# Kernel tuning notes

Hardware: AMD Instinct MI355X
Metric: run time of the kernel (lower is better)

## Reference

```python
import jax, jax.numpy as jnp
import numpy as np

N_NODES = 3_000_000  # divisible by 3 (x.view(-1, 3))
N_EDGES = 48_000_000  # avg degree 16


def setup_inputs() -> dict:
    key = jax.random.key(0)
    ks = jax.random.split(key, 8)
    x = jax.random.normal(ks[0], (N_NODES, 1), dtype=jnp.float32)
    edge_index = jax.random.randint(ks[1], (2, N_EDGES), 0, N_NODES, dtype=jnp.int64)
    # SAGEConv(1, 1, bias=False): lin_l applied to aggregated neighbors, lin_r to root
    W_l = jax.random.normal(ks[2], (1, 1), dtype=jnp.float32)
    W_r = jax.random.normal(ks[3], (1, 1), dtype=jnp.float32)
    # nn.Sequential(Linear(1,2), ReLU, Linear(2,1)) with default biases
    W1 = jax.random.normal(ks[4], (2, 1), dtype=jnp.float32)
    b1 = jax.random.normal(ks[5], (2,), dtype=jnp.float32)
    W2 = jax.random.normal(ks[6], (1, 2), dtype=jnp.float32)
    b2 = jax.random.normal(ks[7], (1,), dtype=jnp.float32)
    return {"x": x, "edge_index": edge_index, "W_l": W_l, "W_r": W_r,
            "W1": W1, "b1": b1, "W2": W2, "b2": b2}


def reference(x, edge_index, W_l, W_r, W1, b1, W2, b2):
    src, dst = edge_index[0], edge_index[1]
    # sum-aggregate messages x_j from source nodes onto target nodes
    agg = jax.ops.segment_sum(x[src], dst, num_segments=N_NODES)  # [N, 1]
    # SAGEConv: lin_l(agg) + lin_r(x)
    h = agg @ W_l.T + x @ W_r.T  # [N, 1]
    # x.view(-1, 3)[:, 0] -> take every 3rd node's feature
    h0 = h.reshape(-1, 3)[:, 0:1]  # [N/3, 1]
    # MLP: Linear(1,2) -> ReLU -> Linear(2,1)
    out = jax.nn.relu(h0 @ W1.T + b1) @ W2.T + b2  # [N/3, 1]
    return out.reshape(-1)
```

## Files before the change

kernel.cpp:

```cpp
#include <hip/hip_runtime.h>


static constexpr int kNodes = 3000000;
static constexpr int kEdges = 48000000;
static constexpr int kOut   = 1000000;

static constexpr int RANGE_LOG = 12;
static constexpr int RANGE     = 1 << RANGE_LOG;
static constexpr int NBINS     = (kOut + RANGE - 1) / RANGE;
static constexpr int NBINS_PAD = 256;
static constexpr int CAP       = 71680;

static constexpr int K1_THREADS = 512;
static constexpr int E_PER_ITER = K1_THREADS * 8;
static constexpr int K1_ITERS   = 16;
static constexpr int E_PER_WG   = E_PER_ITER * K1_ITERS;
static constexpr int K1_GRID    = (kEdges + E_PER_WG - 1) / E_PER_WG;

__global__ __launch_bounds__(512) void scatter_bin3(
    const int* __restrict__ ei,
    const float* __restrict__ x,
    unsigned* __restrict__ count,
    uint2* __restrict__ recs)
{
    __shared__ unsigned hist[NBINS_PAD];
    __shared__ unsigned cur[NBINS_PAD];

    const int tid = threadIdx.x;
    if (tid < NBINS_PAD) hist[tid] = 0;
    __syncthreads();

    const int wgBase = blockIdx.x * E_PER_WG;

    for (int it = 0; it < K1_ITERS; ++it) {
        const int e = wgBase + it * E_PER_ITER + tid * 8;
        if (e < kEdges) {
            const int4 d0 = *reinterpret_cast<const int4*>(ei + kEdges + e);
            const int4 d1 = *reinterpret_cast<const int4*>(ei + kEdges + e + 4);
            const int dd[8] = {d0.x, d0.y, d0.z, d0.w, d1.x, d1.y, d1.z, d1.w};
#pragma unroll
            for (int k = 0; k < 8; ++k) {
                const unsigned d = (unsigned)dd[k];
                const unsigned q = d / 3u;
                if (q * 3u == d) {
                    atomicAdd(&hist[q >> RANGE_LOG], 1u);
                }
            }
        }
    }
    __syncthreads();

    if (tid < NBINS_PAD) {
        const unsigned c = hist[tid];
        unsigned base = 0;
        if (c) base = atomicAdd(&count[tid], c);
        cur[tid] = (unsigned)tid * (unsigned)CAP + base;
    }
    __syncthreads();

    for (int it = 0; it < K1_ITERS; ++it) {
        const int e = wgBase + it * E_PER_ITER + tid * 8;
        if (e < kEdges) {
            const int4 s0 = *reinterpret_cast<const int4*>(ei + e);
            const int4 s1 = *reinterpret_cast<const int4*>(ei + e + 4);
            const int4 d0 = *reinterpret_cast<const int4*>(ei + kEdges + e);
            const int4 d1 = *reinterpret_cast<const int4*>(ei + kEdges + e + 4);

            const int ss[8] = {s0.x, s0.y, s0.z, s0.w, s1.x, s1.y, s1.z, s1.w};
            const int dd[8] = {d0.x, d0.y, d0.z, d0.w, d1.x, d1.y, d1.z, d1.w};

#pragma unroll
            for (int h = 0; h < 2; ++h) {
                unsigned qv[4]; bool ok[4]; float xv[4];
#pragma unroll
                for (int k = 0; k < 4; ++k) {
                    const unsigned d = (unsigned)dd[h * 4 + k];
                    const unsigned q = d / 3u;
                    qv[k] = q;
                    ok[k] = (q * 3u == d);
                    xv[k] = ok[k] ? x[ss[h * 4 + k]] : 0.0f;
                }
#pragma unroll
                for (int k = 0; k < 4; ++k) {
                    if (ok[k]) {
                        const unsigned bin = qv[k] >> RANGE_LOG;
                        const unsigned pos = atomicAdd(&cur[bin], 1u);
                        if (pos < (bin + 1u) * (unsigned)CAP) {
                            uint2 r;
                            r.x = qv[k] & (unsigned)(RANGE - 1);
                            r.y = __float_as_uint(xv[k]);
                            recs[pos] = r;
                        }
                    }
                }
            }
        }
    }
}

__global__ __launch_bounds__(1024) void bin_finalize3(
    const unsigned* __restrict__ count,
    const uint2* __restrict__ recs,
    const float* __restrict__ x,
    const float* __restrict__ Wl,
    const float* __restrict__ Wr,
    const float* __restrict__ W1,
    const float* __restrict__ b1,
    const float* __restrict__ W2,
    const float* __restrict__ b2,
    float* __restrict__ out)
{
    __shared__ float acc[RANGE];

    const int tid = threadIdx.x;
    const int b   = blockIdx.x;

    for (int l = tid; l < RANGE; l += 1024) acc[l] = 0.0f;
    __syncthreads();

    unsigned cnt = count[b];
    if (cnt > (unsigned)CAP) cnt = CAP;
    const uint2* rb = recs + (size_t)b * CAP;

    unsigned i = (unsigned)tid;
    for (; i + 3072u < cnt; i += 4096u) {
        const uint2 r0 = rb[i];
        const uint2 r1 = rb[i + 1024u];
        const uint2 r2 = rb[i + 2048u];
        const uint2 r3 = rb[i + 3072u];
        atomicAdd(&acc[r0.x], __uint_as_float(r0.y));
        atomicAdd(&acc[r1.x], __uint_as_float(r1.y));
        atomicAdd(&acc[r2.x], __uint_as_float(r2.y));
        atomicAdd(&acc[r3.x], __uint_as_float(r3.y));
    }
    for (; i < cnt; i += 1024u) {
        const uint2 r = rb[i];
        atomicAdd(&acc[r.x], __uint_as_float(r.y));
    }
    __syncthreads();

    const float wl  = Wl[0];
    const float wr  = Wr[0];
    const float w10 = W1[0];
    const float w11 = W1[1];
    const float bb0 = b1[0];
    const float bb1 = b1[1];
    const float w20 = W2[0];
    const float w21 = W2[1];
    const float bb2 = b2[0];

    const int j0 = b << RANGE_LOG;
    for (int l = tid; l < RANGE; l += 1024) {
        const int j = j0 + l;
        if (j < kOut) {
            const float h  = acc[l] * wl + x[3 * j] * wr;
            const float t0 = fmaxf(h * w10 + bb0, 0.0f);
            const float t1 = fmaxf(h * w11 + bb1, 0.0f);
            out[j] = t0 * w20 + t1 * w21 + bb2;
        }
    }
}


__global__ __launch_bounds__(256) void edge_scatter(
    const int* __restrict__ ei,
    const float* __restrict__ x,
    float* __restrict__ agg)
{
    const int tid = blockIdx.x * blockDim.x + threadIdx.x;
    const int e = tid * 4;
    if (e >= kEdges) return;

    const int4 s4 = *reinterpret_cast<const int4*>(ei + e);
    const int4 d4 = *reinterpret_cast<const int4*>(ei + kEdges + e);

    const int ss[4] = {s4.x, s4.y, s4.z, s4.w};
    const int dd[4] = {d4.x, d4.y, d4.z, d4.w};

#pragma unroll
    for (int k = 0; k < 4; ++k) {
        const unsigned d = (unsigned)dd[k];
        const unsigned q = d / 3u;
        if (q * 3u == d) {
            atomicAdd(agg + q, x[ss[k]]);
        }
    }
}

__global__ __launch_bounds__(256) void finalize(
    const float* __restrict__ agg,
    const float* __restrict__ x,
    const float* __restrict__ Wl,
    const float* __restrict__ Wr,
    const float* __restrict__ W1,
    const float* __restrict__ b1,
    const float* __restrict__ W2,
    const float* __restrict__ b2,
    float* __restrict__ out)
{
    const int j = blockIdx.x * blockDim.x + threadIdx.x;
    if (j >= kOut) return;

    const float wl  = Wl[0];
    const float wr  = Wr[0];
    const float w10 = W1[0];
    const float w11 = W1[1];
    const float bb0 = b1[0];
    const float bb1 = b1[1];
    const float w20 = W2[0];
    const float w21 = W2[1];
    const float bb2 = b2[0];

    const float h = agg[j] * wl + x[3 * j] * wr;
    const float t0 = fmaxf(h * w10 + bb0, 0.0f);
    const float t1 = fmaxf(h * w11 + bb1, 0.0f);
    out[j] = t0 * w20 + t1 * w21 + bb2;
}

extern "C" void kernel_launch(void* const* d_in, const int* in_sizes, int n_in,
                              void* d_out, int out_size, void* d_ws, size_t ws_size,
                              hipStream_t stream)
{
    const float* x  = (const float*)d_in[0];
    const int*   ei = (const int*)d_in[1];
    const float* Wl = (const float*)d_in[2];
    const float* Wr = (const float*)d_in[3];
    const float* W1 = (const float*)d_in[4];
    const float* b1 = (const float*)d_in[5];
    const float* W2 = (const float*)d_in[6];
    const float* b2 = (const float*)d_in[7];
    float* out = (float*)d_out;

    const size_t cnt_bytes = (size_t)NBINS_PAD * sizeof(unsigned);
    const size_t rec_off   = 4096;
    const size_t rec_bytes = (size_t)NBINS * (size_t)CAP * sizeof(uint2);
    const size_t need      = rec_off + rec_bytes;

    if (ws_size >= need) {
        unsigned* count = (unsigned*)d_ws;
        uint2*    recs  = (uint2*)((char*)d_ws + rec_off);

        hipMemsetAsync(count, 0, cnt_bytes, stream);
        scatter_bin3<<<K1_GRID, K1_THREADS, 0, stream>>>(ei, x, count, recs);
        bin_finalize3<<<NBINS, 1024, 0, stream>>>(count, recs, x, Wl, Wr, W1, b1, W2, b2, out);
    } else {
        float* agg = (float*)d_ws;
        hipMemsetAsync(agg, 0, kOut * sizeof(float), stream);
        const int nThreads = kEdges / 4;
        edge_scatter<<<nThreads / 256, 256, 0, stream>>>(ei, x, agg);
        finalize<<<(kOut + 255) / 256, 256, 0, stream>>>(agg, x, Wl, Wr, W1, b1, W2, b2, out);
    }
}
```

Baseline: 981.7 us.

## Replace two-pass histogram binning with per-workgroup private bins and atomic overflow

```diff
diff --git a/kernel.cpp b/kernel.cpp
--- a/kernel.cpp
+++ b/kernel.cpp
@@ -7,60 +7,40 @@
 
 static constexpr int RANGE_LOG = 12;
 static constexpr int RANGE     = 1 << RANGE_LOG;
-static constexpr int NBINS     = (kOut + RANGE - 1) / RANGE;
+static constexpr int NBINS     = 245;
 static constexpr int NBINS_PAD = 256;
-static constexpr int CAP       = 71680;
-
+
+static constexpr int K1_WGS     = 750;
 static constexpr int K1_THREADS = 512;
+static constexpr int E_PER_WG   = kEdges / K1_WGS;
 static constexpr int E_PER_ITER = K1_THREADS * 8;
-static constexpr int K1_ITERS   = 16;
-static constexpr int E_PER_WG   = E_PER_ITER * K1_ITERS;
-static constexpr int K1_GRID    = (kEdges + E_PER_WG - 1) / E_PER_WG;
-
-__global__ __launch_bounds__(512) void scatter_bin3(
+static constexpr int K1_ITERS   = (E_PER_WG + E_PER_ITER - 1) / E_PER_ITER;
+
+static constexpr unsigned CAP_A = 140;
+static constexpr unsigned CAP_B = 92;
+
+__global__ __launch_bounds__(512) void scatter_sp(
     const int* __restrict__ ei,
     const float* __restrict__ x,
-    unsigned* __restrict__ count,
-    uint2* __restrict__ recs)
-{
-    __shared__ unsigned hist[NBINS_PAD];
+    const unsigned CAP,
+    unsigned* __restrict__ counts,
+    uint2* __restrict__ recs,
+    float* __restrict__ agg)
+{
     __shared__ unsigned cur[NBINS_PAD];
 
     const int tid = threadIdx.x;
-    if (tid < NBINS_PAD) hist[tid] = 0;
-    __syncthreads();
-
-    const int wgBase = blockIdx.x * E_PER_WG;
+    if (tid < NBINS_PAD) cur[tid] = 0;
+    __syncthreads();
+
+    const int wg = blockIdx.x;
+    const int wgBase = wg * E_PER_WG;
+    const unsigned wgRec = (unsigned)wg * (unsigned)NBINS;
 
     for (int it = 0; it < K1_ITERS; ++it) {
-        const int e = wgBase + it * E_PER_ITER + tid * 8;
-        if (e < kEdges) {
-            const int4 d0 = *reinterpret_cast<const int4*>(ei + kEdges + e);
-            const int4 d1 = *reinterpret_cast<const int4*>(ei + kEdges + e + 4);
-            const int dd[8] = {d0.x, d0.y, d0.z, d0.w, d1.x, d1.y, d1.z, d1.w};
-#pragma unroll
-            for (int k = 0; k < 8; ++k) {
-                const unsigned d = (unsigned)dd[k];
-                const unsigned q = d / 3u;
-                if (q * 3u == d) {
-                    atomicAdd(&hist[q >> RANGE_LOG], 1u);
-                }
-            }
-        }
-    }
-    __syncthreads();
-
-    if (tid < NBINS_PAD) {
-        const unsigned c = hist[tid];
-        unsigned base = 0;
-        if (c) base = atomicAdd(&count[tid], c);
-        cur[tid] = (unsigned)tid * (unsigned)CAP + base;
-    }
-    __syncthreads();
-
-    for (int it = 0; it < K1_ITERS; ++it) {
-        const int e = wgBase + it * E_PER_ITER + tid * 8;
-        if (e < kEdges) {
+        const int off = it * E_PER_ITER + tid * 8;
+        if (off < E_PER_WG) {
+            const int e = wgBase + off;
             const int4 s0 = *reinterpret_cast<const int4*>(ei + e);
             const int4 s1 = *reinterpret_cast<const int4*>(ei + e + 4);
             const int4 d0 = *reinterpret_cast<const int4*>(ei + kEdges + e);
@@ -85,22 +65,28 @@
                     if (ok[k]) {
                         const unsigned bin = qv[k] >> RANGE_LOG;
                         const unsigned pos = atomicAdd(&cur[bin], 1u);
-                        if (pos < (bin + 1u) * (unsigned)CAP) {
+                        if (pos < CAP) {
                             uint2 r;
                             r.x = qv[k] & (unsigned)(RANGE - 1);
                             r.y = __float_as_uint(xv[k]);
-                            recs[pos] = r;
+                            recs[(size_t)(wgRec + bin) * CAP + pos] = r;
+                        } else {
+                            atomicAdd(&agg[qv[k]], xv[k]);
                         }
                     }
                 }
             }
         }
     }
-}
-
-__global__ __launch_bounds__(1024) void bin_finalize3(
-    const unsigned* __restrict__ count,
+    __syncthreads();
+    if (tid < NBINS) counts[wg * NBINS_PAD + tid] = min(cur[tid], CAP);
+}
+
+__global__ __launch_bounds__(1024) void finalize_sp(
+    const unsigned* __restrict__ counts,
     const uint2* __restrict__ recs,
+    const unsigned CAP,
+    const float* __restrict__ agg,
     const float* __restrict__ x,
     const float* __restrict__ Wl,
     const float* __restrict__ Wr,
@@ -111,31 +97,32 @@
     float* __restrict__ out)
 {
     __shared__ float acc[RANGE];
+    __shared__ unsigned scnt[K1_WGS];
 
     const int tid = threadIdx.x;
     const int b   = blockIdx.x;
 
     for (int l = tid; l < RANGE; l += 1024) acc[l] = 0.0f;
-    __syncthreads();
-
-    unsigned cnt = count[b];
-    if (cnt > (unsigned)CAP) cnt = CAP;
-    const uint2* rb = recs + (size_t)b * CAP;
-
-    unsigned i = (unsigned)tid;
-    for (; i + 3072u < cnt; i += 4096u) {
-        const uint2 r0 = rb[i];
-        const uint2 r1 = rb[i + 1024u];
-        const uint2 r2 = rb[i + 2048u];
-        const uint2 r3 = rb[i + 3072u];
-        atomicAdd(&acc[r0.x], __uint_as_float(r0.y));
-        atomicAdd(&acc[r1.x], __uint_as_float(r1.y));
-        atomicAdd(&acc[r2.x], __uint_as_float(r2.y));
-        atomicAdd(&acc[r3.x], __uint_as_float(r3.y));
-    }
-    for (; i < cnt; i += 1024u) {
-        const uint2 r = rb[i];
-        atomicAdd(&acc[r.x], __uint_as_float(r.y));
+    if (tid < K1_WGS) scnt[tid] = counts[tid * NBINS_PAD + b];
+    __syncthreads();
+
+    const int wave = tid >> 6;
+    const int lane = tid & 63;
+
+    for (int s = wave; s < K1_WGS; s += 16) {
+        const unsigned cnt = scnt[s];
+        const uint2* base = recs + (size_t)((unsigned)s * (unsigned)NBINS + (unsigned)b) * CAP;
+        unsigned i = (unsigned)lane;
+        for (; i + 64u < cnt; i += 128u) {
+            const uint2 r0 = base[i];
+            const uint2 r1 = base[i + 64u];
+            atomicAdd(&acc[r0.x], __uint_as_float(r0.y));
+            atomicAdd(&acc[r1.x], __uint_as_float(r1.y));
+        }
+        if (i < cnt) {
+            const uint2 r = base[i];
+            atomicAdd(&acc[r.x], __uint_as_float(r.y));
+        }
     }
     __syncthreads();
 
@@ -153,7 +140,8 @@
     for (int l = tid; l < RANGE; l += 1024) {
         const int j = j0 + l;
         if (j < kOut) {
-            const float h  = acc[l] * wl + x[3 * j] * wr;
+            const float a  = acc[l] + agg[j];
+            const float h  = a * wl + x[3 * j] * wr;
             const float t0 = fmaxf(h * w10 + bb0, 0.0f);
             const float t1 = fmaxf(h * w11 + bb1, 0.0f);
             out[j] = t0 * w20 + t1 * w21 + bb2;
@@ -231,18 +219,28 @@
     const float* b2 = (const float*)d_in[7];
     float* out = (float*)d_out;
 
-    const size_t cnt_bytes = (size_t)NBINS_PAD * sizeof(unsigned);
-    const size_t rec_off   = 4096;
-    const size_t rec_bytes = (size_t)NBINS * (size_t)CAP * sizeof(uint2);
-    const size_t need      = rec_off + rec_bytes;
-
-    if (ws_size >= need) {
-        unsigned* count = (unsigned*)d_ws;
-        uint2*    recs  = (uint2*)((char*)d_ws + rec_off);
-
-        hipMemsetAsync(count, 0, cnt_bytes, stream);
-        scatter_bin3<<<K1_GRID, K1_THREADS, 0, stream>>>(ei, x, count, recs);
-        bin_finalize3<<<NBINS, 1024, 0, stream>>>(count, recs, x, Wl, Wr, W1, b1, W2, b2, out);
+    const size_t rec_off = 8192;
+
+    const size_t recsA = (size_t)K1_WGS * NBINS * CAP_A * sizeof(uint2);
+    const size_t recsB = (size_t)K1_WGS * NBINS * CAP_B * sizeof(uint2);
+    const size_t agg_bytes = (size_t)kOut * sizeof(float);
+    const size_t cnt_bytes = (size_t)K1_WGS * NBINS_PAD * sizeof(unsigned);
+
+    const size_t needA = rec_off + recsA + agg_bytes + cnt_bytes;
+    const size_t needB = rec_off + recsB + agg_bytes + cnt_bytes;
+
+    if (ws_size >= needB) {
+        const unsigned CAP     = (ws_size >= needA) ? CAP_A : CAP_B;
+        const size_t   recsz   = (ws_size >= needA) ? recsA : recsB;
+
+        uint2*    recs   = (uint2*)((char*)d_ws + rec_off);
+        float*    agg    = (float*)((char*)d_ws + rec_off + recsz);
+        unsigned* counts = (unsigned*)((char*)d_ws + rec_off + recsz + agg_bytes);
+
+        hipMemsetAsync(agg, 0, agg_bytes, stream);
+        scatter_sp<<<K1_WGS, K1_THREADS, 0, stream>>>(ei, x, CAP, counts, recs, agg);
+        finalize_sp<<<NBINS, 1024, 0, stream>>>(counts, recs, CAP, agg, x,
+                                                Wl, Wr, W1, b1, W2, b2, out);
     } else {
         float* agg = (float*)d_ws;
         hipMemsetAsync(agg, 0, kOut * sizeof(float), stream);
```

Result: faster. 945.3 us (-3.7%).
